# Optimization experiments

Measured on AMD Instinct MI355X. Metric: run time of the kernel, lower is better.

## Reference

```python
import jax, jax.numpy as jnp
import numpy as np

V, E, H, K = 8000, 100, 64, 17  # vocab, embed, hidden, num_tags (fixed by source)
B, T = 256, 512


def setup_inputs() -> dict:
    key = jax.random.key(0)
    ks = jax.random.split(key, 16)
    g = lambda i, shape: (jax.random.normal(ks[i], shape, jnp.float32) * 0.1)
    data = jax.random.randint(ks[0], (B, T), 0, V).astype(jnp.int32)
    mask = jnp.ones((B, T), dtype=bool)
    return {
        "data": data,
        "mask": mask,
        "emb": g(1, (V, E)),
        # PyTorch LSTM layout: gates stacked [i, f, g, o] along dim 0
        "Wih_f": g(2, (4 * H, E)), "Whh_f": g(3, (4 * H, H)),
        "bih_f": g(4, (4 * H,)), "bhh_f": g(5, (4 * H,)),
        "Wih_b": g(6, (4 * H, E)), "Whh_b": g(7, (4 * H, H)),
        "bih_b": g(8, (4 * H,)), "bhh_b": g(9, (4 * H,)),
        "W_out": g(10, (K, 2 * H)), "b_out": g(11, (K,)),
        "trans": g(12, (K, K)),            # trans[i, j] = score of i -> j
        "start_trans": g(13, (K,)),
        "end_trans": g(14, (K,)),
    }


def _lstm_dir(x, Wih, Whh, bih, bhh, reverse):
    # x: [B, T, E] -> hidden states [B, T, H]
    Bx, Tx, _ = x.shape
    Hx = Whh.shape[1]
    xs = jnp.swapaxes(x, 0, 1)  # [T, B, E]

    def step(carry, xt):
        h, c = carry
        gates = xt @ Wih.T + h @ Whh.T + bih + bhh  # [B, 4H]
        i, f, g, o = jnp.split(gates, 4, axis=-1)
        c = jax.nn.sigmoid(f) * c + jax.nn.sigmoid(i) * jnp.tanh(g)
        h = jax.nn.sigmoid(o) * jnp.tanh(c)
        return (h, c), h

    init = (jnp.zeros((Bx, Hx), x.dtype), jnp.zeros((Bx, Hx), x.dtype))
    _, hs = jax.lax.scan(step, init, xs, reverse=reverse)
    return jnp.swapaxes(hs, 0, 1)  # [B, T, H]


def _emissions(data, emb, Wih_f, Whh_f, bih_f, bhh_f, Wih_b, Whh_b, bih_b, bhh_b, W_out, b_out):
    x = emb[data]                                         # [B, T, E]
    hf = _lstm_dir(x, Wih_f, Whh_f, bih_f, bhh_f, False)  # [B, T, H]
    hb = _lstm_dir(x, Wih_b, Whh_b, bih_b, bhh_b, True)   # [B, T, H]
    h = jnp.concatenate([hf, hb], axis=-1)                # [B, T, 2H]
    return h @ W_out.T + b_out                            # [B, T, K]


def _viterbi(emission, mask, trans, start_trans, end_trans):
    Bx, Tx, Kx = emission.shape
    score = start_trans[None, :] + emission[:, 0]         # [B, K]
    em = jnp.swapaxes(emission, 0, 1)[1:]                 # [T-1, B, K]
    mk = jnp.swapaxes(mask, 0, 1)[1:]                     # [T-1, B]
    ident = jnp.arange(Kx)

    def step(score, inp):
        emit_t, m_t = inp
        # cand[b, i, j] = score[b, i] + trans[i, j] + emit_t[b, j]
        cand = score[:, :, None] + trans[None] + emit_t[:, None, :]
        new = cand.max(axis=1)
        bp = cand.argmax(axis=1)
        score = jnp.where(m_t[:, None], new, score)
        bp = jnp.where(m_t[:, None], bp, ident[None, :])
        return score, bp

    score, bps = jax.lax.scan(step, score, (em, mk))       # bps: [T-1, B, K]
    final = score + end_trans[None, :]
    best_score = final.max(axis=1)                         # [B]
    last = final.argmax(axis=1)                            # [B]

    def back(tag, bp_t):
        prev = jnp.take_along_axis(bp_t, tag[:, None], axis=1)[:, 0]
        return prev, prev

    _, prevs = jax.lax.scan(back, last, bps, reverse=True)  # [T-1, B]
    paths = jnp.concatenate([prevs, last[None, :]], axis=0).T  # [B, T]
    return best_score, paths


def reference(data, mask, emb, Wih_f, Whh_f, bih_f, bhh_f, Wih_b, Whh_b, bih_b, bhh_b,
              W_out, b_out, trans, start_trans, end_trans):
    emission = _emissions(data, emb, Wih_f, Whh_f, bih_f, bhh_f,
                          Wih_b, Whh_b, bih_b, bhh_b, W_out, b_out)
    return _viterbi(emission, mask, trans, start_trans, end_trans)
```

## Files before the change

### kernel.cpp

```cpp
#include <hip/hip_runtime.h>
#include <hip/hip_bf16.h>

typedef unsigned int u32;
typedef unsigned char u8;

#define B_ 256
#define T_ 512
#define E_ 100
#define H_ 64
#define K_ 17
#define V_ 8000

#define WS_G     0
#define WS_H     16384000
#define WS_EMIT  83492864
#define WS_BP    92405760
#define WS_LAST  96600064

__global__ __launch_bounds__(256) void k1_build_G(
    const float* __restrict__ emb,
    const float* __restrict__ Wih_f,
    const float* __restrict__ bih_f,
    const float* __restrict__ bhh_f,
    const float* __restrict__ Wih_b,
    const float* __restrict__ bih_b,
    const float* __restrict__ bhh_b,
    float* __restrict__ G)
{
  __shared__ float xl[32 * E_];
  int v0 = blockIdx.x * 32;
  int dir = blockIdx.y;
  int tid = threadIdx.x;
  const float* Wih = dir ? Wih_b : Wih_f;
  const float* bih = dir ? bih_b : bih_f;
  const float* bhh = dir ? bhh_b : bhh_f;

  for (int i = tid; i < 32 * E_; i += 256) xl[i] = emb[v0 * E_ + i];

  int u = tid >> 2, g = tid & 3;
  int row = (g << 6) + u;
  float4 A4[25];
  {
    const float4* wp = reinterpret_cast<const float4*>(Wih + row * E_);
#pragma unroll
    for (int q = 0; q < 25; ++q) A4[q] = wp[q];
  }
  float bias = __fadd_rn(bih[row], bhh[row]);
  __syncthreads();

  float* Gd = G + (size_t)dir * V_ * 256;
  for (int vi = 0; vi < 32; ++vi) {
    const float* xp = &xl[vi * E_];
    float a0 = bias, a1 = 0.f, a2 = 0.f, a3 = 0.f;
#pragma unroll
    for (int q = 0; q < 25; ++q) {
      float4 w4 = A4[q];
      float4 x4 = *reinterpret_cast<const float4*>(&xp[4 * q]);
      a0 = fmaf(w4.x, x4.x, a0);
      a1 = fmaf(w4.y, x4.y, a1);
      a2 = fmaf(w4.z, x4.z, a2);
      a3 = fmaf(w4.w, x4.w, a3);
    }
    Gd[(v0 + vi) * 256 + tid] = (a0 + a1) + (a2 + a3);
  }
}

__global__ __launch_bounds__(512, 4) void k2_lstm(
    const int* __restrict__ data,
    const float* __restrict__ G,
    const float* __restrict__ Whh_f,
    const float* __restrict__ Whh_b,
    float* __restrict__ hout)
{
  __shared__ __align__(16) float hls[2][64];
  int bid = blockIdx.x;
  int b = bid & 255;
  int dir = bid >> 8;
  int tid = threadIdx.x;
  int w = tid >> 6, l = tid & 63;
  int ul = l >> 3;
  int r = l & 7;
  int g = r >> 1;
  int half = r & 1;
  int u = (w << 3) + ul;
  int row = (g << 6) + u;
  int gidx = (u << 2) + g;
  const float* Whh = dir ? Whh_b : Whh_f;

  float W[32];
  {
    const float4* wp = reinterpret_cast<const float4*>(Whh + row * 64 + half * 32);
#pragma unroll
    for (int q = 0; q < 8; ++q) {
      float4 v = wp[q];
      W[q * 4 + 0] = v.x;
      W[q * 4 + 1] = v.y;
      W[q * 4 + 2] = v.z;
      W[q * 4 + 3] = v.w;
    }
  }
  const float L2E = 1.4426950408889634f;
  float zs = (g == 2) ? (-2.0f * L2E) : (-L2E);
  float ma = (g == 2) ? 2.0f : 1.0f;
  float aa = (g == 2) ? -1.0f : 0.0f;

  if (tid < 64) hls[0][tid] = 0.0f;
  float c = 0.0f;
  const int* tokp = data + b * T_;
  const float* Gd = G + (size_t)dir * V_ * 256;
  float* hob = hout + ((size_t)(dir * B_ + b)) * T_ * H_;

  float g0 = Gd[(size_t)tokp[dir ? (T_ - 1) : 0] * 256 + gidx];
  float g1 = Gd[(size_t)tokp[dir ? (T_ - 2) : 1] * 256 + gidx];
  __syncthreads();

  int cur = 0;
  for (int s = 0; s < T_; ++s) {
    int tt = dir ? (T_ - 1 - s) : s;
    float g2 = 0.0f;
    if (s < T_ - 2) {
      int ttn = dir ? (T_ - 3 - s) : (s + 2);
      g2 = Gd[(size_t)tokp[ttn] * 256 + gidx];
    }
    const float* hb_ = hls[cur] + (half << 5);
    float a0 = (half == 0) ? g0 : 0.0f;
    float a1 = 0.f, a2 = 0.f, a3 = 0.f;
#pragma unroll
    for (int k4 = 0; k4 < 8; ++k4) {
      float4 h4 = *reinterpret_cast<const float4*>(&hb_[k4 * 4]);
      a0 = fmaf(W[k4 * 4 + 0], h4.x, a0);
      a1 = fmaf(W[k4 * 4 + 1], h4.y, a1);
      a2 = fmaf(W[k4 * 4 + 2], h4.z, a2);
      a3 = fmaf(W[k4 * 4 + 3], h4.w, a3);
    }
    float part = (a0 + a1) + (a2 + a3);
    float full = part + __shfl_xor(part, 1, 64);
    float ex = __builtin_amdgcn_exp2f(full * zs);
    float sg = __builtin_amdgcn_rcpf(1.0f + ex);
    float act = fmaf(ma, sg, aa);
    int base = l & 56;
    float iv = __shfl(act, base + 0, 64);
    float fv = __shfl(act, base + 2, 64);
    float gv = __shfl(act, base + 4, 64);
    float ov = __shfl(act, base + 6, 64);
    c = __fadd_rn(__fmul_rn(fv, c), __fmul_rn(iv, gv));
    float tc = fmaf(2.0f,
                    __builtin_amdgcn_rcpf(1.0f + __builtin_amdgcn_exp2f(c * (-2.0f * L2E))),
                    -1.0f);
    float hn = __fmul_rn(ov, tc);
    if (r == 0) {
      hls[cur ^ 1][u] = hn;
      hob[tt * H_ + u] = hn;
    }
    __syncthreads();
    cur ^= 1;
    g0 = g1; g1 = g2;
  }
}

__global__ __launch_bounds__(256) void k3_emit(
    const float* __restrict__ hbuf,
    const float* __restrict__ W_out,
    const float* __restrict__ b_out,
    float* __restrict__ emit)
{
  __shared__ float hl[64][132];
  __shared__ float Wl[17][132];
  int tid = threadIdx.x;
  int p0 = blockIdx.x * 64;
  const float* hf = hbuf;
  const float* hb = hbuf + (size_t)B_ * T_ * H_;
#pragma unroll
  for (int i = 0; i < 4; ++i) {
    int idx = tid + i * 256;
    int pos = idx >> 4, e4 = idx & 15;
    float4 v = reinterpret_cast<const float4*>(hf + (size_t)p0 * 64)[idx];
    *reinterpret_cast<float4*>(&hl[pos][e4 * 4]) = v;
    float4 v2 = reinterpret_cast<const float4*>(hb + (size_t)p0 * 64)[idx];
    *reinterpret_cast<float4*>(&hl[pos][64 + e4 * 4]) = v2;
  }
  for (int i = tid; i < 17 * 128; i += 256) {
    int k = i >> 7, e = i & 127;
    Wl[k][e] = W_out[i];
  }
  __syncthreads();

  int pos = tid >> 2, ks = tid & 3;
  float acc[5] = {0.f, 0.f, 0.f, 0.f, 0.f};
#pragma unroll
  for (int e4 = 0; e4 < 32; ++e4) {
    float4 x4 = *reinterpret_cast<const float4*>(&hl[pos][e4 * 4]);
#pragma unroll
    for (int kk = 0; kk < 5; ++kk) {
      int k = ks + kk * 4;
      if (k < K_) {
        float4 w4 = *reinterpret_cast<const float4*>(&Wl[k][e4 * 4]);
        acc[kk] = fmaf(x4.x, w4.x, acc[kk]);
        acc[kk] = fmaf(x4.y, w4.y, acc[kk]);
        acc[kk] = fmaf(x4.z, w4.z, acc[kk]);
        acc[kk] = fmaf(x4.w, w4.w, acc[kk]);
      }
    }
  }
#pragma unroll
  for (int kk = 0; kk < 5; ++kk) {
    int k = ks + kk * 4;
    if (k < K_)
      emit[(size_t)(p0 + pos) * K_ + k] = __fadd_rn(acc[kk], b_out[k]);
  }
}

#define AMAX(vA, iA, vB, iB) { bool tk_ = (vB) > (vA); if (tk_) { vA = (vB); iA = (iB); } }

__global__ __launch_bounds__(64) void k4_viterbi(
    const float* __restrict__ emit,
    const float* __restrict__ trans,
    const float* __restrict__ start_trans,
    const float* __restrict__ end_trans,
    u8* __restrict__ bp,
    int* __restrict__ last,
    float* __restrict__ out)
{
  int b = blockIdx.x;
  int l = threadIdx.x;
  int ic = l >> 5;
  int hbase = l & 32;
  int j = l & 31;
  int jc = (j < K_) ? j : 0;
  int i0 = ic ? 9 : 0;
  int cnt = ic ? 8 : 9;
  float tr[9];
#pragma unroll
  for (int q = 0; q < 9; ++q)
    tr[q] = (q < cnt) ? trans[(i0 + q) * K_ + jc] : -__builtin_inff();
  const float* eb = emit + (size_t)b * T_ * K_;
  float endt = end_trans[jc];
  float s = __fadd_rn(start_trans[jc], eb[jc]);
  u8* bpb = bp + (size_t)b * T_ * 32;
  float e0 = eb[K_ + jc];
  float e1 = eb[2 * K_ + jc];

  for (int t = 1; t < T_; ++t) {
    float ej = e0;
    e0 = e1;
    if (t + 2 < T_) e1 = eb[(size_t)(t + 2) * K_ + jc];
    float sv[9];
#pragma unroll
    for (int q = 0; q < 9; ++q) sv[q] = __shfl(s, hbase + i0 + q, 64);
    float cd[9];
#pragma unroll
    for (int q = 0; q < 9; ++q) cd[q] = __fadd_rn(__fadd_rn(sv[q], tr[q]), ej);
    float v01 = cd[0]; int x01 = i0;     AMAX(v01, x01, cd[1], i0 + 1);
    float v23 = cd[2]; int x23 = i0 + 2; AMAX(v23, x23, cd[3], i0 + 3);
    float v45 = cd[4]; int x45 = i0 + 4; AMAX(v45, x45, cd[5], i0 + 5);
    float v67 = cd[6]; int x67 = i0 + 6; AMAX(v67, x67, cd[7], i0 + 7);
    AMAX(v01, x01, v23, x23);
    AMAX(v45, x45, v67, x67);
    AMAX(v01, x01, v45, x45);
    AMAX(v01, x01, cd[8], i0 + 8);
    float m = v01; int idx = x01;
    float m2 = __shfl_xor(m, 32, 64);
    int idx2 = __shfl_xor(idx, 32, 64);
    bool take = (m2 > m) || ((m2 == m) && (idx2 < idx));
    if (take) { m = m2; idx = idx2; }
    s = m;
    if (ic == 0 && j < K_) bpb[(size_t)(t - 1) * 32 + j] = (u8)idx;
  }
  float fin = __fadd_rn(s, endt);
  float bm = __shfl(fin, hbase, 64);
  int bi = 0;
#pragma unroll
  for (int jj = 1; jj < K_; ++jj) {
    float v = __shfl(fin, hbase + jj, 64);
    if (v > bm) { bm = v; bi = jj; }
  }
  if (l == 0) {
    out[b] = bm;
    last[b] = bi;
    out[256 + (size_t)b * T_ + (T_ - 1)] = (float)bi;
  }
}

__global__ __launch_bounds__(64) void k5_backtrace(
    const u8* __restrict__ bp,
    const int* __restrict__ last,
    float* __restrict__ out)
{
  int b = blockIdx.x * 64 + threadIdx.x;
  const u8* base = bp + (size_t)b * T_ * 32;
  int tag = last[b];
  float* ob = out + 256 + (size_t)b * T_;
  uint4 A0[8], A1[8];
  u32 B0[8], B1[8];
#pragma unroll
  for (int q = 0; q < 8; ++q) {
    const u8* p = base + (size_t)(510 - q) * 32;
    A0[q] = *reinterpret_cast<const uint4*>(p);
    B0[q] = *reinterpret_cast<const u32*>(p + 16);
  }
  int t0 = 510;
  for (int pair = 0; pair < 32; ++pair) {
#pragma unroll
    for (int q = 0; q < 8; ++q) {
      int tn = t0 - 8 - q;
      if (tn >= 0) {
        const u8* p = base + (size_t)tn * 32;
        A1[q] = *reinterpret_cast<const uint4*>(p);
        B1[q] = *reinterpret_cast<const u32*>(p + 16);
      }
    }
#pragma unroll
    for (int q = 0; q < 8; ++q) {
      int t = t0 - q;
      if (t >= 0) {
        uint4 Av = A0[q]; u32 Bw = B0[q];
        u32 dw = (tag < 8) ? ((tag < 4) ? Av.x : Av.y) : ((tag < 12) ? Av.z : Av.w);
        dw = (tag < 16) ? dw : Bw;
        tag = (int)((dw >> ((tag & 3) * 8)) & 0xffu);
        ob[t] = (float)tag;
      }
    }
#pragma unroll
    for (int q = 0; q < 8; ++q) {
      int tn = t0 - 16 - q;
      if (tn >= 0) {
        const u8* p = base + (size_t)tn * 32;
        A0[q] = *reinterpret_cast<const uint4*>(p);
        B0[q] = *reinterpret_cast<const u32*>(p + 16);
      }
    }
#pragma unroll
    for (int q = 0; q < 8; ++q) {
      int t = t0 - 8 - q;
      if (t >= 0) {
        uint4 Av = A1[q]; u32 Bw = B1[q];
        u32 dw = (tag < 8) ? ((tag < 4) ? Av.x : Av.y) : ((tag < 12) ? Av.z : Av.w);
        dw = (tag < 16) ? dw : Bw;
        tag = (int)((dw >> ((tag & 3) * 8)) & 0xffu);
        ob[t] = (float)tag;
      }
    }
    t0 -= 16;
  }
}

extern "C" void kernel_launch(void* const* d_in, const int* in_sizes, int n_in,
                              void* d_out, int out_size, void* d_ws, size_t ws_size,
                              hipStream_t stream) {
  const int*   data  = (const int*)d_in[0];
  const float* emb   = (const float*)d_in[2];
  const float* Wih_f = (const float*)d_in[3];
  const float* Whh_f = (const float*)d_in[4];
  const float* bih_f = (const float*)d_in[5];
  const float* bhh_f = (const float*)d_in[6];
  const float* Wih_b = (const float*)d_in[7];
  const float* Whh_b = (const float*)d_in[8];
  const float* bih_b = (const float*)d_in[9];
  const float* bhh_b = (const float*)d_in[10];
  const float* W_out = (const float*)d_in[11];
  const float* b_out = (const float*)d_in[12];
  const float* trans = (const float*)d_in[13];
  const float* start_trans = (const float*)d_in[14];
  const float* end_trans   = (const float*)d_in[15];

  char* ws = (char*)d_ws;
  float* G    = (float*)(ws + WS_G);
  float* hbuf = (float*)(ws + WS_H);
  float* emit = (float*)(ws + WS_EMIT);
  u8*    bp   = (u8*)(ws + WS_BP);
  int*   lastp = (int*)(ws + WS_LAST);
  float* out = (float*)d_out;

  k1_build_G<<<dim3(250, 2), 256, 0, stream>>>(emb, Wih_f, bih_f, bhh_f,
                                               Wih_b, bih_b, bhh_b, G);
  k2_lstm<<<512, 512, 0, stream>>>(data, G, Whh_f, Whh_b, hbuf);
  k3_emit<<<2048, 256, 0, stream>>>(hbuf, W_out, b_out, emit);
  k4_viterbi<<<256, 64, 0, stream>>>(emit, trans, start_trans, end_trans,
                                     bp, lastp, out);
  k5_backtrace<<<4, 64, 0, stream>>>(bp, lastp, out);
}
```

Baseline: 716.5 us.

## Remap LSTM recurrence so each thread computes all four gates of one unit

After: 661.4 us. 7.7% less time.

```diff
diff --git a/kernel.cpp b/kernel.cpp
--- a/kernel.cpp
+++ b/kernel.cpp
@@ -16,6 +16,15 @@
 #define WS_EMIT  83492864
 #define WS_BP    92405760
 #define WS_LAST  96600064
+
+__device__ __forceinline__ float qp_xor1(float v) {
+  int r = __builtin_amdgcn_update_dpp(0, __builtin_bit_cast(int, v), 0xB1, 0xF, 0xF, true);
+  return __builtin_bit_cast(float, r);
+}
+__device__ __forceinline__ float qp_xor2(float v) {
+  int r = __builtin_amdgcn_update_dpp(0, __builtin_bit_cast(int, v), 0x4E, 0xF, 0xF, true);
+  return __builtin_bit_cast(float, r);
+}
 
 __global__ __launch_bounds__(256) void k1_build_G(
     const float* __restrict__ emb,
@@ -65,7 +74,7 @@
   }
 }
 
-__global__ __launch_bounds__(512, 4) void k2_lstm(
+__global__ __launch_bounds__(256, 2) void k2_lstm(
     const int* __restrict__ data,
     const float* __restrict__ G,
     const float* __restrict__ Whh_f,
@@ -78,83 +87,82 @@
   int dir = bid >> 8;
   int tid = threadIdx.x;
   int w = tid >> 6, l = tid & 63;
-  int ul = l >> 3;
-  int r = l & 7;
-  int g = r >> 1;
-  int half = r & 1;
-  int u = (w << 3) + ul;
-  int row = (g << 6) + u;
-  int gidx = (u << 2) + g;
+  int ul = l >> 2;
+  int kq = l & 3;
+  int u = (w << 4) + ul;
   const float* Whh = dir ? Whh_b : Whh_f;
 
-  float W[32];
-  {
-    const float4* wp = reinterpret_cast<const float4*>(Whh + row * 64 + half * 32);
-#pragma unroll
-    for (int q = 0; q < 8; ++q) {
+  float W[4][16];
+#pragma unroll
+  for (int g = 0; g < 4; ++g) {
+    const float4* wp = reinterpret_cast<const float4*>(Whh + ((g << 6) + u) * 64 + (kq << 4));
+#pragma unroll
+    for (int q = 0; q < 4; ++q) {
       float4 v = wp[q];
-      W[q * 4 + 0] = v.x;
-      W[q * 4 + 1] = v.y;
-      W[q * 4 + 2] = v.z;
-      W[q * 4 + 3] = v.w;
-    }
-  }
-  const float L2E = 1.4426950408889634f;
-  float zs = (g == 2) ? (-2.0f * L2E) : (-L2E);
-  float ma = (g == 2) ? 2.0f : 1.0f;
-  float aa = (g == 2) ? -1.0f : 0.0f;
-
+      W[g][q * 4 + 0] = v.x;
+      W[g][q * 4 + 1] = v.y;
+      W[g][q * 4 + 2] = v.z;
+      W[g][q * 4 + 3] = v.w;
+    }
+  }
   if (tid < 64) hls[0][tid] = 0.0f;
   float c = 0.0f;
   const int* tokp = data + b * T_;
   const float* Gd = G + (size_t)dir * V_ * 256;
   float* hob = hout + ((size_t)(dir * B_ + b)) * T_ * H_;
-
-  float g0 = Gd[(size_t)tokp[dir ? (T_ - 1) : 0] * 256 + gidx];
-  float g1 = Gd[(size_t)tokp[dir ? (T_ - 2) : 1] * 256 + gidx];
+  const float L2E = 1.4426950408889634f;
+
+  float4 gq0 = *reinterpret_cast<const float4*>(&Gd[(size_t)tokp[dir ? (T_ - 1) : 0] * 256 + (u << 2)]);
+  float4 gq1 = *reinterpret_cast<const float4*>(&Gd[(size_t)tokp[dir ? (T_ - 2) : 1] * 256 + (u << 2)]);
   __syncthreads();
 
   int cur = 0;
   for (int s = 0; s < T_; ++s) {
     int tt = dir ? (T_ - 1 - s) : s;
-    float g2 = 0.0f;
+    float4 gq2 = make_float4(0.f, 0.f, 0.f, 0.f);
     if (s < T_ - 2) {
       int ttn = dir ? (T_ - 3 - s) : (s + 2);
-      g2 = Gd[(size_t)tokp[ttn] * 256 + gidx];
-    }
-    const float* hb_ = hls[cur] + (half << 5);
-    float a0 = (half == 0) ? g0 : 0.0f;
-    float a1 = 0.f, a2 = 0.f, a3 = 0.f;
-#pragma unroll
-    for (int k4 = 0; k4 < 8; ++k4) {
-      float4 h4 = *reinterpret_cast<const float4*>(&hb_[k4 * 4]);
-      a0 = fmaf(W[k4 * 4 + 0], h4.x, a0);
-      a1 = fmaf(W[k4 * 4 + 1], h4.y, a1);
-      a2 = fmaf(W[k4 * 4 + 2], h4.z, a2);
-      a3 = fmaf(W[k4 * 4 + 3], h4.w, a3);
-    }
-    float part = (a0 + a1) + (a2 + a3);
-    float full = part + __shfl_xor(part, 1, 64);
-    float ex = __builtin_amdgcn_exp2f(full * zs);
-    float sg = __builtin_amdgcn_rcpf(1.0f + ex);
-    float act = fmaf(ma, sg, aa);
-    int base = l & 56;
-    float iv = __shfl(act, base + 0, 64);
-    float fv = __shfl(act, base + 2, 64);
-    float gv = __shfl(act, base + 4, 64);
-    float ov = __shfl(act, base + 6, 64);
-    c = __fadd_rn(__fmul_rn(fv, c), __fmul_rn(iv, gv));
-    float tc = fmaf(2.0f,
-                    __builtin_amdgcn_rcpf(1.0f + __builtin_amdgcn_exp2f(c * (-2.0f * L2E))),
-                    -1.0f);
-    float hn = __fmul_rn(ov, tc);
-    if (r == 0) {
+      gq2 = *reinterpret_cast<const float4*>(&Gd[(size_t)tokp[ttn] * 256 + (u << 2)]);
+    }
+    const float* hq = hls[cur] + (kq << 4);
+    float4 h4[4];
+#pragma unroll
+    for (int q = 0; q < 4; ++q) h4[q] = *reinterpret_cast<const float4*>(&hq[q * 4]);
+    float acc[4];
+#pragma unroll
+    for (int g = 0; g < 4; ++g) {
+      float b0 = 0.f, b1 = 0.f, b2 = 0.f, b3 = 0.f;
+#pragma unroll
+      for (int q = 0; q < 4; ++q) {
+        b0 = fmaf(W[g][q * 4 + 0], h4[q].x, b0);
+        b1 = fmaf(W[g][q * 4 + 1], h4[q].y, b1);
+        b2 = fmaf(W[g][q * 4 + 2], h4[q].z, b2);
+        b3 = fmaf(W[g][q * 4 + 3], h4[q].w, b3);
+      }
+      acc[g] = (b0 + b1) + (b2 + b3);
+    }
+    float t0 = acc[0] + qp_xor1(acc[0]); float f0 = t0 + qp_xor2(t0);
+    float t1 = acc[1] + qp_xor1(acc[1]); float f1 = t1 + qp_xor2(t1);
+    float t2 = acc[2] + qp_xor1(acc[2]); float f2 = t2 + qp_xor2(t2);
+    float t3 = acc[3] + qp_xor1(acc[3]); float f3 = t3 + qp_xor2(t3);
+    float xi = f0 + gq0.x;
+    float xf = f1 + gq0.y;
+    float xg = f2 + gq0.z;
+    float xo = f3 + gq0.w;
+    float si = __builtin_amdgcn_rcpf(1.0f + __builtin_amdgcn_exp2f(xi * (-L2E)));
+    float sf = __builtin_amdgcn_rcpf(1.0f + __builtin_amdgcn_exp2f(xf * (-L2E)));
+    float tg = fmaf(2.0f, __builtin_amdgcn_rcpf(1.0f + __builtin_amdgcn_exp2f(xg * (-2.0f * L2E))), -1.0f);
+    float so = __builtin_amdgcn_rcpf(1.0f + __builtin_amdgcn_exp2f(xo * (-L2E)));
+    c = __fadd_rn(__fmul_rn(sf, c), __fmul_rn(si, tg));
+    float tc = fmaf(2.0f, __builtin_amdgcn_rcpf(1.0f + __builtin_amdgcn_exp2f(c * (-2.0f * L2E))), -1.0f);
+    float hn = __fmul_rn(so, tc);
+    if (kq == 0) {
       hls[cur ^ 1][u] = hn;
       hob[tt * H_ + u] = hn;
     }
-    __syncthreads();
+    asm volatile("s_waitcnt lgkmcnt(0)\n\ts_barrier" ::: "memory");
     cur ^= 1;
-    g0 = g1; g1 = g2;
+    gq0 = gq1; gq1 = gq2;
   }
 }
 
@@ -237,13 +245,15 @@
   float endt = end_trans[jc];
   float s = __fadd_rn(start_trans[jc], eb[jc]);
   u8* bpb = bp + (size_t)b * T_ * 32;
-  float e0 = eb[K_ + jc];
-  float e1 = eb[2 * K_ + jc];
+  float er0 = eb[1 * K_ + jc];
+  float er1 = eb[2 * K_ + jc];
+  float er2 = eb[3 * K_ + jc];
+  float er3 = eb[4 * K_ + jc];
 
   for (int t = 1; t < T_; ++t) {
-    float ej = e0;
-    e0 = e1;
-    if (t + 2 < T_) e1 = eb[(size_t)(t + 2) * K_ + jc];
+    float ej = er0;
+    er0 = er1; er1 = er2; er2 = er3;
+    if (t + 4 < T_) er3 = eb[(size_t)(t + 4) * K_ + jc];
     float sv[9];
 #pragma unroll
     for (int q = 0; q < 9; ++q) sv[q] = __shfl(s, hbase + i0 + q, 64);
@@ -373,7 +383,7 @@
 
   k1_build_G<<<dim3(250, 2), 256, 0, stream>>>(emb, Wih_f, bih_f, bhh_f,
                                                Wih_b, bih_b, bhh_b, G);
-  k2_lstm<<<512, 512, 0, stream>>>(data, G, Whh_f, Whh_b, hbuf);
+  k2_lstm<<<512, 256, 0, stream>>>(data, G, Whh_f, Whh_b, hbuf);
   k3_emit<<<2048, 256, 0, stream>>>(hbuf, W_out, b_out, emit);
   k4_viterbi<<<256, 64, 0, stream>>>(emit, trans, start_trans, end_trans,
                                      bp, lastp, out);
```
